# Kernel optimization log

Measured on AMD Instinct MI355X. Metric: run time of the kernel, lower is better.

The kernel has to match this reference:

```python
import jax, jax.numpy as jnp
import numpy as np
import math

B, S, D, H = 2, 2048, 1024, 16
DH = D // H

def setup_inputs() -> dict:
    key = jax.random.key(0)
    ks = jax.random.split(key, 12)
    s = 1.0 / math.sqrt(D)
    return {
        "q": jax.random.normal(ks[0], (B, S, D), jnp.float32),
        "k": jax.random.normal(ks[1], (B, S, D), jnp.float32),
        "v": jax.random.normal(ks[2], (B, S, D), jnp.float32),
        "mask": jnp.tril(jnp.ones((S, S), dtype=bool)),  # causal mask
        "Wq": jax.random.normal(ks[3], (D, D), jnp.float32) * s,
        "bq": jnp.zeros((D,), jnp.float32),
        "Wk": jax.random.normal(ks[4], (D, D), jnp.float32) * s,
        "bk": jnp.zeros((D,), jnp.float32),
        "Wv": jax.random.normal(ks[5], (D, D), jnp.float32) * s,
        "bv": jnp.zeros((D,), jnp.float32),
        "Wo": jax.random.normal(ks[6], (D, D), jnp.float32) * s,
        "bo": jnp.zeros((D,), jnp.float32),
    }

def _split_heads(x):
    b, s, _ = x.shape
    return x.reshape(b, s, H, DH).transpose(0, 2, 1, 3)  # [B,H,S,DH]

def reference(q, k, v, mask, Wq, bq, Wk, bk, Wv, bv, Wo, bo):
    qh = _split_heads(q @ Wq.T + bq)
    kh = _split_heads(k @ Wk.T + bk)
    vh = _split_heads(v @ Wv.T + bv)
    scale = 1.0 / math.sqrt(DH)
    scores = jnp.einsum('bhqd,bhkd->bhqk', qh, kh) * scale  # [B,H,S,S]
    scores = jnp.where(mask[None, None, :, :], scores, -jnp.inf)
    attn = jax.nn.softmax(scores, axis=-1)
    out = jnp.einsum('bhqk,bhkd->bhqd', attn, vh)  # [B,H,S,DH]
    out = out.transpose(0, 2, 1, 3).reshape(B, S, D)  # combine heads
    return out @ Wo.T + bo
```

## Files before the change

### kernel.cpp

```cpp
#include <hip/hip_runtime.h>

typedef unsigned int u32;
typedef unsigned short u16;
typedef __attribute__((ext_vector_type(8))) short bf16x8;
typedef __attribute__((ext_vector_type(8))) u16 u16x8;
typedef __attribute__((ext_vector_type(4))) u16 u16x4;
typedef __attribute__((ext_vector_type(4))) float f32x4;
typedef __attribute__((ext_vector_type(2))) u32 u32x2;

#define AS1 __attribute__((address_space(1)))
#define AS3 __attribute__((address_space(3)))

__device__ __forceinline__ void gload_lds16(const void* g, void* l) {
  __builtin_amdgcn_global_load_lds((const AS1 u32*)g, (AS3 u32*)l, 16, 0, 0);
}

__device__ __forceinline__ u16 f2bf(float f) {
  union { float f; u32 u; } x; x.f = f;
  u32 u = x.u;
  return (u16)((u + 0x7fffu + ((u >> 16) & 1u)) >> 16);
}

__device__ __forceinline__ u32 cvt_pk_bf16(float lo, float hi) {
  u32 r;
  asm("v_cvt_pk_bf16_f32 %0, %1, %2" : "=v"(r) : "v"(lo), "v"(hi));
  return r;
}

__device__ __forceinline__ float fexp2(float x) {
  float r;
  asm("v_exp_f32 %0, %1" : "=v"(r) : "v"(x));
  return r;
}

__global__ __launch_bounds__(256) void convert_all(
    const float* __restrict__ q, const float* __restrict__ k, const float* __restrict__ v,
    const float* __restrict__ wq, const float* __restrict__ wk,
    const float* __restrict__ wv, const float* __restrict__ wo,
    u16* __restrict__ dst)
{
  int b = blockIdx.x, t = threadIdx.x;
  const float* sp; size_t lb;
  if (b < 6144) {
    sp = (b < 2048) ? q : ((b < 4096) ? k : v);
    lb = (size_t)(b & 2047) * 2048;
  } else {
    int w = (b - 6144) >> 9;
    sp = (w == 0) ? wq : ((w == 1) ? wk : ((w == 2) ? wv : wo));
    lb = (size_t)((b - 6144) & 511) * 2048;
  }
  lb += (size_t)t * 8;
  f32x4 f0 = *(const f32x4*)(sp + lb);
  f32x4 f1 = *(const f32x4*)(sp + lb + 4);
  u16x8 o;
  o[0]=f2bf(f0[0]); o[1]=f2bf(f0[1]); o[2]=f2bf(f0[2]); o[3]=f2bf(f0[3]);
  o[4]=f2bf(f1[0]); o[5]=f2bf(f1[1]); o[6]=f2bf(f1[2]); o[7]=f2bf(f1[3]);
  *(u16x8*)(dst + (size_t)b*2048 + (size_t)t*8) = o;
}

__global__ __launch_bounds__(512, 2) void gemm_qkv(
    const u16* __restrict__ Xall,
    const u16* __restrict__ Wall,
    const float* __restrict__ bq, const float* __restrict__ bk, const float* __restrict__ bv,
    u16* __restrict__ Cqk, u16* __restrict__ VT)
{
  __shared__ __align__(16) u16 lds[49152];
  const int t = threadIdx.x;
  const int w = t >> 6, l = t & 63;
  const int c = l & 15, g = l >> 4;
  const int u = blockIdx.x;
  const int lid = (u & 7) * 24 + (u >> 3);
  const int by = lid / 12, rest = lid % 12;
  const int which = rest >> 2, ntl = rest & 3;
  const int m0 = by * 256, n0 = ntl * 256;
  const u16* A  = Xall + (size_t)which * 4194304;
  const u16* Bw = Wall + (size_t)which * 1048576;
  const int wr = w >> 2, wc = w & 3;

  const int srow = w*16 + (l >> 2);
  const int schk = l & 3;
  const int sswz = (schk ^ (srow & 3) ^ ((srow >> 2) & 3)) << 3;
  const u16* Asrc0 = A  + (size_t)(m0 + srow)*1024       + sswz;
  const u16* Asrc1 = A  + (size_t)(m0 + 128 + srow)*1024 + sswz;
  const u16* Bsrc0 = Bw + (size_t)(n0 + srow)*1024       + sswz;
  const u16* Bsrc1 = Bw + (size_t)(n0 + 128 + srow)*1024 + sswz;
  const int wbase = w * 512;

#define QKV_STAGE(j) do { \
    const int bo_ = ((j) % 3) * 16384; const int ko_ = (j) << 5; \
    gload_lds16(Asrc0 + ko_, &lds[bo_ + wbase]); \
    gload_lds16(Asrc1 + ko_, &lds[bo_ + 4096 + wbase]); \
    gload_lds16(Bsrc0 + ko_, &lds[bo_ + 8192 + wbase]); \
    gload_lds16(Bsrc1 + ko_, &lds[bo_ + 12288 + wbase]); \
  } while (0)

  const int fswz = (g ^ (c & 3) ^ (c >> 2)) << 3;
  const int abase = (wr*128 + c)*32 + fswz;
  const int bbase = 8192 + (wc*64 + c)*32 + fswz;

  f32x4 acc[8][4] = {};

  QKV_STAGE(0);
  QKV_STAGE(1);
  asm volatile("s_waitcnt vmcnt(4)" ::: "memory");
  __builtin_amdgcn_s_barrier();
  __builtin_amdgcn_sched_barrier(0);

#pragma unroll
  for (int tstep = 0; tstep < 32; ++tstep) {
    if (tstep + 2 < 32) QKV_STAGE(tstep + 2);
    const int bo = (tstep % 3) * 16384;
    bf16x8 af[8], bf[4];
#pragma unroll
    for (int mf = 0; mf < 8; ++mf)
      af[mf] = *(const bf16x8*)&lds[bo + abase + mf*512];
#pragma unroll
    for (int nf = 0; nf < 4; ++nf)
      bf[nf] = *(const bf16x8*)&lds[bo + bbase + nf*512];
    __builtin_amdgcn_s_setprio(1);
#pragma unroll
    for (int mf = 0; mf < 8; ++mf)
#pragma unroll
      for (int nf = 0; nf < 4; ++nf)
        acc[mf][nf] = __builtin_amdgcn_mfma_f32_16x16x32_bf16(af[mf], bf[nf], acc[mf][nf], 0, 0, 0);
    __builtin_amdgcn_s_setprio(0);
    if (tstep + 2 < 32) asm volatile("s_waitcnt vmcnt(4)" ::: "memory");
    else                asm volatile("s_waitcnt vmcnt(0)" ::: "memory");
    __builtin_amdgcn_s_barrier();
    __builtin_amdgcn_sched_barrier(0);
  }
#undef QKV_STAGE

  const float* bias = (which == 0) ? bq : ((which == 1) ? bk : bv);
  if (which < 2) {
#pragma unroll
    for (int mf = 0; mf < 8; ++mf)
#pragma unroll
      for (int nf = 0; nf < 4; ++nf) {
        int row = m0 + wr*128 + mf*16 + g*4;
        int col = n0 + wc*64 + nf*16 + c;
        float bv_ = bias[col];
        int colg = which*1024 + col;
#pragma unroll
        for (int r = 0; r < 4; ++r)
          Cqk[(size_t)(row+r)*2048 + colg] = f2bf(acc[mf][nf][r] + bv_);
      }
  } else {
#pragma unroll
    for (int mf = 0; mf < 8; ++mf)
#pragma unroll
      for (int nf = 0; nf < 4; ++nf) {
        int row = m0 + wr*128 + mf*16 + g*4;
        int col = n0 + wc*64 + nf*16 + c;
        float bv_ = bias[col];
        int bb2 = row >> 11, s = row & 2047;
        int hh = col >> 6, dh = col & 63;
        u16x4 pk;
#pragma unroll
        for (int r = 0; r < 4; ++r) pk[r] = f2bf(acc[mf][nf][r] + bv_);
        *(u16x4*)&VT[((size_t)(((bb2<<4)+hh)<<6) + dh)*2048 + s] = pk;
      }
  }
}

__global__ __launch_bounds__(256) void gemm_out(
    const u16* __restrict__ A, const u16* __restrict__ Bw,
    const float* __restrict__ bias, float* __restrict__ C)
{
  __shared__ __align__(16) u16 As[128*64];
  __shared__ __align__(16) u16 Bs[64*64];
  const int t = threadIdx.x;
  const int wid = t >> 6, l = t & 63;
  const int l4 = l >> 4, l15 = l & 15;
  const int m0 = blockIdx.y * 128, n0 = blockIdx.x * 64;
  const int wr = wid >> 1, wc = wid & 1;
  const int arow = t >> 3, achk = t & 7;

  f32x4 acc[4][2] = {};

  for (int k0 = 0; k0 < 1024; k0 += 64) {
    __syncthreads();
#pragma unroll
    for (int i = 0; i < 4; ++i) {
      int row = i*32 + arow;
      gload_lds16(A + (size_t)(m0+row)*1024 + k0 + ((achk ^ (row&7)) << 3),
                  &As[i*2048 + wid*512]);
    }
#pragma unroll
    for (int i = 0; i < 2; ++i) {
      int row = i*32 + arow;
      gload_lds16(Bw + (size_t)(n0+row)*1024 + k0 + ((achk ^ (row&7)) << 3),
                  &Bs[i*2048 + wid*512]);
    }
    __syncthreads();
#pragma unroll
    for (int kh = 0; kh < 2; ++kh) {
      bf16x8 af[4], bf[2];
#pragma unroll
      for (int mf = 0; mf < 4; ++mf) {
        int row = wr*64 + mf*16 + l15;
        int ch = (kh*4 + l4) ^ (row & 7);
        af[mf] = *(const bf16x8*)&As[row*64 + ch*8];
      }
#pragma unroll
      for (int nf = 0; nf < 2; ++nf) {
        int row = wc*32 + nf*16 + l15;
        int ch = (kh*4 + l4) ^ (row & 7);
        bf[nf] = *(const bf16x8*)&Bs[row*64 + ch*8];
      }
#pragma unroll
      for (int mf = 0; mf < 4; ++mf)
#pragma unroll
        for (int nf = 0; nf < 2; ++nf)
          acc[mf][nf] = __builtin_amdgcn_mfma_f32_16x16x32_bf16(af[mf], bf[nf], acc[mf][nf], 0, 0, 0);
    }
  }
#pragma unroll
  for (int mf = 0; mf < 4; ++mf)
#pragma unroll
    for (int nf = 0; nf < 2; ++nf) {
      int row = m0 + wr*64 + mf*16 + l4*4;
      int col = n0 + wc*32 + nf*16 + l15;
      float bv = bias[col];
#pragma unroll
      for (int r = 0; r < 4; ++r)
        C[(size_t)(row+r)*1024 + col] = acc[mf][nf][r] + bv;
    }
}

__device__ __forceinline__ void stage_kv(u16* lds, const u16* Kt, const u16* Vt,
                                         int buf, int wid) {
#pragma unroll
  for (int ii = 0; ii < 2; ++ii)
    gload_lds16(Kt + (size_t)ii*32*2048, &lds[4096 + buf*4096 + ii*2048 + wid*512]);
#pragma unroll
  for (int ii = 0; ii < 2; ++ii)
    gload_lds16(Vt + (size_t)ii*32*2048, &lds[12288 + buf*4096 + ii*2048 + wid*512]);
}

__device__ __forceinline__ void attn_phase(
    u16* lds, const u16* Qg, const u16* Ka, const u16* Va,
    int q0, int kt0, int nkv, bool maskLast,
    int wid, int g, int c, int arow, int achk, int pbase, int cs,
    float& MI, float& LI, f32x4 (&o)[4])
{
  const float SC = 0.18033688f;
#pragma unroll
  for (int i = 0; i < 2; ++i) {
    int row = i*32 + arow;
    gload_lds16(Qg + (size_t)(q0+row)*2048 + ((achk ^ (row&7)) << 3),
                &lds[i*2048 + wid*512]);
  }
  const u16* Kt = Ka + (size_t)kt0 * (64*2048);
  const u16* Vt = Va + kt0 * 64;
  stage_kv(lds, Kt, Vt, 0, wid);
  asm volatile("s_waitcnt vmcnt(0)" ::: "memory");
  __builtin_amdgcn_s_barrier();
  __builtin_amdgcn_sched_barrier(0);

  bf16x8 qf[2];
#pragma unroll
  for (int kh = 0; kh < 2; ++kh) {
    int row = wid*16 + c;
    int ch = (kh*4 + g) ^ (row & 7);
    qf[kh] = *(const bf16x8*)&lds[row*64 + ch*8];
  }

  float mi = -INFINITY, li = 0.f;
#pragma unroll
  for (int df = 0; df < 4; ++df) o[df] = f32x4{0.f, 0.f, 0.f, 0.f};

  for (int i = 0; i < nkv; ++i) {
    if (i + 1 < nkv) {
      Kt += 64*2048; Vt += 64;
      stage_kv(lds, Kt, Vt, (i+1)&1, wid);
    }
    const u16* Kb = &lds[4096  + (i&1)*4096];
    const u16* Vb = &lds[12288 + (i&1)*4096];

    f32x4 sT[4] = {};
    __builtin_amdgcn_s_setprio(1);
#pragma unroll
    for (int kh = 0; kh < 2; ++kh) {
      bf16x8 kf[4];
#pragma unroll
      for (int nf = 0; nf < 4; ++nf) {
        int row = nf*16 + c;
        int ch = (kh*4 + g) ^ (c & 7);
        kf[nf] = *(const bf16x8*)&Kb[row*64 + ch*8];
      }
#pragma unroll
      for (int nf = 0; nf < 4; ++nf)
        sT[nf] = __builtin_amdgcn_mfma_f32_16x16x32_bf16(kf[nf], qf[kh], sT[nf], 0,0,0);
    }
    __builtin_amdgcn_s_setprio(0);

    if (maskLast && i == nkv - 1) {
#pragma unroll
      for (int nf = 0; nf < 4; ++nf)
#pragma unroll
        for (int r = 0; r < 4; ++r)
          if (nf*16 + g*4 + r > wid*16 + c) sT[nf][r] = -INFINITY;
    }

    float mx = fmaxf(fmaxf(sT[0][0], sT[0][1]), fmaxf(sT[0][2], sT[0][3]));
#pragma unroll
    for (int nf = 1; nf < 4; ++nf)
      mx = fmaxf(mx, fmaxf(fmaxf(sT[nf][0], sT[nf][1]), fmaxf(sT[nf][2], sT[nf][3])));
    mx = fmaxf(mx, __shfl_xor(mx, 16, 64));
    mx = fmaxf(mx, __shfl_xor(mx, 32, 64));
    float mn = fmaxf(mi, mx * SC);
    float corr = fexp2(mi - mn);
    float sum = 0.f;
#pragma unroll
    for (int nf = 0; nf < 4; ++nf)
#pragma unroll
      for (int r = 0; r < 4; ++r) {
        float pv = fexp2(fmaf(sT[nf][r], SC, -mn));
        sT[nf][r] = pv;
        sum += pv;
      }
    sum += __shfl_xor(sum, 16, 64);
    sum += __shfl_xor(sum, 32, 64);
    li = li * corr + sum;
    mi = mn;

#pragma unroll
    for (int df = 0; df < 4; ++df) {
      o[df][0] *= corr; o[df][1] *= corr;
      o[df][2] *= corr; o[df][3] *= corr;
    }

#pragma unroll
    for (int nf = 0; nf < 4; ++nf) {
      u32x2 ww;
      ww[0] = cvt_pk_bf16(sT[nf][0], sT[nf][1]);
      ww[1] = cvt_pk_bf16(sT[nf][2], sT[nf][3]);
      int ch = (2*nf + (g >> 1)) ^ cs;
      *(u32x2*)&lds[pbase + c*64 + ch*8 + (g & 1)*4] = ww;
    }
    asm volatile("s_waitcnt lgkmcnt(0)" ::: "memory");
    __builtin_amdgcn_sched_barrier(0);

    __builtin_amdgcn_s_setprio(1);
#pragma unroll
    for (int kh = 0; kh < 2; ++kh) {
      bf16x8 pfr, vf[4];
      {
        int ch = (kh*4 + g) ^ cs;
        pfr = *(const bf16x8*)&lds[pbase + c*64 + ch*8];
      }
#pragma unroll
      for (int df = 0; df < 4; ++df) {
        int d = df*16 + c;
        int ch = (kh*4 + g) ^ (d & 7);
        vf[df] = *(const bf16x8*)&Vb[d*64 + ch*8];
      }
#pragma unroll
      for (int df = 0; df < 4; ++df)
        o[df] = __builtin_amdgcn_mfma_f32_16x16x32_bf16(vf[df], pfr, o[df], 0,0,0);
    }
    __builtin_amdgcn_s_setprio(0);

    asm volatile("s_waitcnt vmcnt(0)" ::: "memory");
    __builtin_amdgcn_s_barrier();
    __builtin_amdgcn_sched_barrier(0);
  }
  MI = mi; LI = li;
}

__device__ __forceinline__ void store_partial(
    float* __restrict__ part, int slot, int s,
    int wid, int g, int c, float mi, float li, const f32x4 (&o)[4])
{
  float* po = part + (size_t)(slot*2 + s) * 4224;
  int q = wid*16 + c;
#pragma unroll
  for (int df = 0; df < 4; ++df)
    *(f32x4*)&po[q*64 + df*16 + g*4] = o[df];
  if (g == 0) { po[4096 + q] = mi; po[4160 + q] = li; }
}

__global__ __launch_bounds__(256, 4) void attn_fwd(
    const u16* __restrict__ QK, const u16* __restrict__ VT,
    u16* __restrict__ AO, float* __restrict__ part)
{
  __shared__ __align__(16) u16 lds[20480];
  const int t = threadIdx.x;
  const int wid = t >> 6, l = t & 63;
  const int g = l >> 4, c = l & 15;
  const int u = blockIdx.x;
  const int lid = (u & 7) * 128 + (u >> 3);
  const int gx = lid & 31, h = (lid >> 5) & 15, b = lid >> 9;
  const int p = gx >> 1, s = gx & 1;
  const u16* Qg  = QK + (size_t)b * 2048 * 2048 + (size_t)h * 64;
  const u16* Kg  = Qg + 1024;
  const u16* VTg = VT + (size_t)(((b << 4) + h) << 6) * 2048;
  const int arow = t >> 3, achk = t & 7;
  const int pbase = wid * 1024;
  const int cs = (c & 7) ^ ((c >> 3) << 2);
  const u16* Ka = Kg  + (size_t)arow*2048 + ((achk ^ (arow & 7)) << 3);
  const u16* Va = VTg + (size_t)arow*2048 + ((achk ^ (arow & 7)) << 3);
  const int slot = ((b*16 + h)*16 + p);

  float mi, li; f32x4 o[4];

  if (s == 0) {
    attn_phase(lds, Qg, Ka, Va, p*64, 0, p+1, true,
               wid, g, c, arow, achk, pbase, cs, mi, li, o);
    {
      float nr = 1.f / li;
      int row = p*64 + wid*16 + c;
      size_t rb = ((size_t)b*2048 + row)*1024 + h*64;
#pragma unroll
      for (int df = 0; df < 4; ++df) {
        u16x4 pk;
        pk[0] = f2bf(o[df][0] * nr); pk[1] = f2bf(o[df][1] * nr);
        pk[2] = f2bf(o[df][2] * nr); pk[3] = f2bf(o[df][3] * nr);
        *(u16x4*)&AO[rb + df*16 + g*4] = pk;
      }
    }
    attn_phase(lds, Qg, Ka, Va, (31-p)*64, 0, 16-p, false,
               wid, g, c, arow, achk, pbase, cs, mi, li, o);
    store_partial(part, slot, 0, wid, g, c, mi, li, o);
  } else {
    attn_phase(lds, Qg, Ka, Va, (31-p)*64, 16-p, 16, true,
               wid, g, c, arow, achk, pbase, cs, mi, li, o);
    store_partial(part, slot, 1, wid, g, c, mi, li, o);
  }
}

__global__ __launch_bounds__(256) void attn_merge(
    const float* __restrict__ part, u16* __restrict__ AO)
{
  int slot = blockIdx.x;
  int p = slot & 15;
  int h = (slot >> 4) & 15;
  int b = slot >> 8;
  const float* p0 = part + (size_t)slot * 8448;
  const float* p1 = p0 + 4224;
  int t = threadIdx.x;
  int r = t >> 2, c0 = (t & 3) * 16;
  float m0 = p0[4096 + r], m1 = p1[4096 + r];
  float l0 = p0[4160 + r], l1 = p1[4160 + r];
  float m = fmaxf(m0, m1);
  float e0 = exp2f(m0 - m), e1 = exp2f(m1 - m);
  float rl = 1.f / (l0*e0 + l1*e1);
  e0 *= rl; e1 *= rl;
  const f32x4* a0 = (const f32x4*)(p0 + r*64 + c0);
  const f32x4* a1 = (const f32x4*)(p1 + r*64 + c0);
  u16x8 w0, w1;
#pragma unroll
  for (int q4 = 0; q4 < 4; ++q4) {
    f32x4 x = a0[q4], y = a1[q4];
#pragma unroll
    for (int j = 0; j < 4; ++j) {
      u16 bf = f2bf(x[j]*e0 + y[j]*e1);
      if (q4 < 2) w0[q4*4+j] = bf; else w1[(q4-2)*4+j] = bf;
    }
  }
  int qrow = (31 - p)*64 + r;
  size_t ab = ((size_t)b*2048 + qrow)*1024 + h*64 + c0;
  *(u16x8*)&AO[ab]     = w0;
  *(u16x8*)&AO[ab + 8] = w1;
}

extern "C" void kernel_launch(void* const* d_in, const int* in_sizes, int n_in,
                              void* d_out, int out_size, void* d_ws, size_t ws_size,
                              hipStream_t stream)
{
  const float* q  = (const float*)d_in[0];
  const float* k  = (const float*)d_in[1];
  const float* v  = (const float*)d_in[2];
  const float* Wq = (const float*)d_in[4];
  const float* bq = (const float*)d_in[5];
  const float* Wk = (const float*)d_in[6];
  const float* bk = (const float*)d_in[7];
  const float* Wv = (const float*)d_in[8];
  const float* bv = (const float*)d_in[9];
  const float* Wo = (const float*)d_in[10];
  const float* bo = (const float*)d_in[11];
  float* out = (float*)d_out;

  u16* ws   = (u16*)d_ws;
  u16* qb   = ws;
  u16* Wqb  = ws + 12582912;
  u16* Wob  = ws + 15728640;
  u16* QKp  = ws + 16777216;
  u16* VTp  = ws + 25165824;
  u16* AO   = ws + 29360128;

  convert_all<<<8192, 256, 0, stream>>>(q, k, v, Wq, Wk, Wv, Wo, qb);

  gemm_qkv<<<192, 512, 0, stream>>>(qb, Wqb, bq, bk, bv, QKp, VTp);

  attn_fwd<<<1024, 256, 0, stream>>>(QKp, VTp, AO, (float*)d_ws);

  attn_merge<<<512, 256, 0, stream>>>((const float*)d_ws, AO);

  dim3 g1(16, 32);
  gemm_out<<<g1, 256, 0, stream>>>(AO, Wob, bo, out);
}
```

Baseline: 114.7 us.

## Shrink QKV GEMM tiles to 128x128 and add lazy softmax rescaling in attention

The QKV projection GEMM moves from 192 blocks of 512 threads with 256x256 tiles to 768 blocks of 256 threads with 128x128 tiles, using half the LDS and fewer accumulators. This aims to fill more compute units and raise occupancy, at the cost of less data reuse per tile. Separately, the attention softmax now skips the max-reduction shuffles and the rescaling of the output accumulator unless some lane's max exceeds the running max by a threshold. It also defers the cross-lane row-sum reduction until each phase finishes, which removes per-iteration shuffles but lets exponentials grow up to 2^8 in the interim.

Measured after the change: 109.0 us. 1.05x faster.

```diff
diff --git a/kernel.cpp b/kernel.cpp
--- a/kernel.cpp
+++ b/kernel.cpp
@@ -58,47 +58,46 @@
   *(u16x8*)(dst + (size_t)b*2048 + (size_t)t*8) = o;
 }
 
-__global__ __launch_bounds__(512, 2) void gemm_qkv(
+__global__ __launch_bounds__(256, 3) void gemm_qkv(
     const u16* __restrict__ Xall,
     const u16* __restrict__ Wall,
     const float* __restrict__ bq, const float* __restrict__ bk, const float* __restrict__ bv,
     u16* __restrict__ Cqk, u16* __restrict__ VT)
 {
-  __shared__ __align__(16) u16 lds[49152];
+  __shared__ __align__(16) u16 lds[24576];
   const int t = threadIdx.x;
-  const int w = t >> 6, l = t & 63;
+  const int wid = t >> 6, l = t & 63;
   const int c = l & 15, g = l >> 4;
   const int u = blockIdx.x;
-  const int lid = (u & 7) * 24 + (u >> 3);
-  const int by = lid / 12, rest = lid % 12;
-  const int which = rest >> 2, ntl = rest & 3;
-  const int m0 = by * 256, n0 = ntl * 256;
+  const int lid = (u & 7) * 96 + (u >> 3);
+  const int which = lid >> 8;
+  const int r5 = lid & 255;
+  const int m0 = (r5 >> 3) * 128, n0 = (r5 & 7) * 128;
   const u16* A  = Xall + (size_t)which * 4194304;
   const u16* Bw = Wall + (size_t)which * 1048576;
-  const int wr = w >> 2, wc = w & 3;
-
-  const int srow = w*16 + (l >> 2);
-  const int schk = l & 3;
-  const int sswz = (schk ^ (srow & 3) ^ ((srow >> 2) & 3)) << 3;
-  const u16* Asrc0 = A  + (size_t)(m0 + srow)*1024       + sswz;
-  const u16* Asrc1 = A  + (size_t)(m0 + 128 + srow)*1024 + sswz;
-  const u16* Bsrc0 = Bw + (size_t)(n0 + srow)*1024       + sswz;
-  const u16* Bsrc1 = Bw + (size_t)(n0 + 128 + srow)*1024 + sswz;
-  const int wbase = w * 512;
+  const int wr = wid >> 1, wc = wid & 1;
+
+  const int srow = wid*16 + (l >> 2);
+  const int sswz = ((l & 3) ^ (srow & 3) ^ ((srow >> 2) & 3)) << 3;
+  const u16* Asrc0 = A  + (size_t)(m0 + srow)*1024      + sswz;
+  const u16* Asrc1 = A  + (size_t)(m0 + 64 + srow)*1024 + sswz;
+  const u16* Bsrc0 = Bw + (size_t)(n0 + srow)*1024      + sswz;
+  const u16* Bsrc1 = Bw + (size_t)(n0 + 64 + srow)*1024 + sswz;
+  const int wbase = wid * 512;
 
 #define QKV_STAGE(j) do { \
-    const int bo_ = ((j) % 3) * 16384; const int ko_ = (j) << 5; \
+    const int bo_ = ((j) % 3) * 8192; const int ko_ = (j) << 5; \
     gload_lds16(Asrc0 + ko_, &lds[bo_ + wbase]); \
-    gload_lds16(Asrc1 + ko_, &lds[bo_ + 4096 + wbase]); \
-    gload_lds16(Bsrc0 + ko_, &lds[bo_ + 8192 + wbase]); \
-    gload_lds16(Bsrc1 + ko_, &lds[bo_ + 12288 + wbase]); \
+    gload_lds16(Asrc1 + ko_, &lds[bo_ + 2048 + wbase]); \
+    gload_lds16(Bsrc0 + ko_, &lds[bo_ + 4096 + wbase]); \
+    gload_lds16(Bsrc1 + ko_, &lds[bo_ + 6144 + wbase]); \
   } while (0)
 
-  const int fswz = (g ^ (c & 3) ^ (c >> 2)) << 3;
-  const int abase = (wr*128 + c)*32 + fswz;
-  const int bbase = 8192 + (wc*64 + c)*32 + fswz;
-
-  f32x4 acc[8][4] = {};
+  const int fswz = (g ^ (c & 3) ^ ((c >> 2) & 3)) << 3;
+  const int abase = (wr*64 + c)*32 + fswz;
+  const int bbase = 4096 + (wc*64 + c)*32 + fswz;
+
+  f32x4 acc[4][4] = {};
 
   QKV_STAGE(0);
   QKV_STAGE(1);
@@ -109,17 +108,17 @@
 #pragma unroll
   for (int tstep = 0; tstep < 32; ++tstep) {
     if (tstep + 2 < 32) QKV_STAGE(tstep + 2);
-    const int bo = (tstep % 3) * 16384;
-    bf16x8 af[8], bf[4];
-#pragma unroll
-    for (int mf = 0; mf < 8; ++mf)
+    const int bo = (tstep % 3) * 8192;
+    bf16x8 af[4], bf[4];
+#pragma unroll
+    for (int mf = 0; mf < 4; ++mf)
       af[mf] = *(const bf16x8*)&lds[bo + abase + mf*512];
 #pragma unroll
     for (int nf = 0; nf < 4; ++nf)
       bf[nf] = *(const bf16x8*)&lds[bo + bbase + nf*512];
     __builtin_amdgcn_s_setprio(1);
 #pragma unroll
-    for (int mf = 0; mf < 8; ++mf)
+    for (int mf = 0; mf < 4; ++mf)
 #pragma unroll
       for (int nf = 0; nf < 4; ++nf)
         acc[mf][nf] = __builtin_amdgcn_mfma_f32_16x16x32_bf16(af[mf], bf[nf], acc[mf][nf], 0, 0, 0);
@@ -134,10 +133,10 @@
   const float* bias = (which == 0) ? bq : ((which == 1) ? bk : bv);
   if (which < 2) {
 #pragma unroll
-    for (int mf = 0; mf < 8; ++mf)
+    for (int mf = 0; mf < 4; ++mf)
 #pragma unroll
       for (int nf = 0; nf < 4; ++nf) {
-        int row = m0 + wr*128 + mf*16 + g*4;
+        int row = m0 + wr*64 + mf*16 + g*4;
         int col = n0 + wc*64 + nf*16 + c;
         float bv_ = bias[col];
         int colg = which*1024 + col;
@@ -147,10 +146,10 @@
       }
   } else {
 #pragma unroll
-    for (int mf = 0; mf < 8; ++mf)
+    for (int mf = 0; mf < 4; ++mf)
 #pragma unroll
       for (int nf = 0; nf < 4; ++nf) {
-        int row = m0 + wr*128 + mf*16 + g*4;
+        int row = m0 + wr*64 + mf*16 + g*4;
         int col = n0 + wc*64 + nf*16 + c;
         float bv_ = bias[col];
         int bb2 = row >> 11, s = row & 2047;
@@ -307,29 +306,29 @@
 #pragma unroll
     for (int nf = 1; nf < 4; ++nf)
       mx = fmaxf(mx, fmaxf(fmaxf(sT[nf][0], sT[nf][1]), fmaxf(sT[nf][2], sT[nf][3])));
-    mx = fmaxf(mx, __shfl_xor(mx, 16, 64));
-    mx = fmaxf(mx, __shfl_xor(mx, 32, 64));
-    float mn = fmaxf(mi, mx * SC);
-    float corr = fexp2(mi - mn);
+    if (!__all(mx * SC <= mi + 8.f)) {
+      float mxr = fmaxf(mx, __shfl_xor(mx, 16, 64));
+      mxr = fmaxf(mxr, __shfl_xor(mxr, 32, 64));
+      float mn = fmaxf(mi, mxr * SC);
+      float corr = fexp2(mi - mn);
+      li *= corr;
+#pragma unroll
+      for (int df = 0; df < 4; ++df) {
+        o[df][0] *= corr; o[df][1] *= corr;
+        o[df][2] *= corr; o[df][3] *= corr;
+      }
+      mi = mn;
+    }
     float sum = 0.f;
 #pragma unroll
     for (int nf = 0; nf < 4; ++nf)
 #pragma unroll
       for (int r = 0; r < 4; ++r) {
-        float pv = fexp2(fmaf(sT[nf][r], SC, -mn));
+        float pv = fexp2(fmaf(sT[nf][r], SC, -mi));
         sT[nf][r] = pv;
         sum += pv;
       }
-    sum += __shfl_xor(sum, 16, 64);
-    sum += __shfl_xor(sum, 32, 64);
-    li = li * corr + sum;
-    mi = mn;
-
-#pragma unroll
-    for (int df = 0; df < 4; ++df) {
-      o[df][0] *= corr; o[df][1] *= corr;
-      o[df][2] *= corr; o[df][3] *= corr;
-    }
+    li += sum;
 
 #pragma unroll
     for (int nf = 0; nf < 4; ++nf) {
@@ -371,14 +370,14 @@
 
 __device__ __forceinline__ void store_partial(
     float* __restrict__ part, int slot, int s,
-    int wid, int g, int c, float mi, float li, const f32x4 (&o)[4])
+    int wid, int g, int c, float mi, float li_tot, const f32x4 (&o)[4])
 {
   float* po = part + (size_t)(slot*2 + s) * 4224;
   int q = wid*16 + c;
 #pragma unroll
   for (int df = 0; df < 4; ++df)
     *(f32x4*)&po[q*64 + df*16 + g*4] = o[df];
-  if (g == 0) { po[4096 + q] = mi; po[4160 + q] = li; }
+  if (g == 0) { po[4096 + q] = mi; po[4160 + q] = li_tot; }
 }
 
 __global__ __launch_bounds__(256, 4) void attn_fwd(
@@ -409,7 +408,9 @@
     attn_phase(lds, Qg, Ka, Va, p*64, 0, p+1, true,
                wid, g, c, arow, achk, pbase, cs, mi, li, o);
     {
-      float nr = 1.f / li;
+      float lt = li + __shfl_xor(li, 16, 64);
+      lt += __shfl_xor(lt, 32, 64);
+      float nr = 1.f / lt;
       int row = p*64 + wid*16 + c;
       size_t rb = ((size_t)b*2048 + row)*1024 + h*64;
 #pragma unroll
@@ -422,11 +423,15 @@
     }
     attn_phase(lds, Qg, Ka, Va, (31-p)*64, 0, 16-p, false,
                wid, g, c, arow, achk, pbase, cs, mi, li, o);
-    store_partial(part, slot, 0, wid, g, c, mi, li, o);
+    float lt = li + __shfl_xor(li, 16, 64);
+    lt += __shfl_xor(lt, 32, 64);
+    store_partial(part, slot, 0, wid, g, c, mi, lt, o);
   } else {
     attn_phase(lds, Qg, Ka, Va, (31-p)*64, 16-p, 16, true,
                wid, g, c, arow, achk, pbase, cs, mi, li, o);
-    store_partial(part, slot, 1, wid, g, c, mi, li, o);
+    float lt = li + __shfl_xor(li, 16, 64);
+    lt += __shfl_xor(lt, 32, 64);
+    store_partial(part, slot, 1, wid, g, c, mi, lt, o);
   }
 }
 
@@ -492,7 +497,7 @@
 
   convert_all<<<8192, 256, 0, stream>>>(q, k, v, Wq, Wk, Wv, Wo, qb);
 
-  gemm_qkv<<<192, 512, 0, stream>>>(qb, Wqb, bq, bk, bv, QKp, VTp);
+  gemm_qkv<<<768, 256, 0, stream>>>(qb, Wqb, bq, bk, bv, QKp, VTp);
 
   attn_fwd<<<1024, 256, 0, stream>>>(QKp, VTp, AO, (float*)d_ws);
 
```
